# Kernel tuning notes

Hardware: AMD Instinct MI355X
Metric: run time of the kernel (lower is better)

## Reference

```python
import jax, jax.numpy as jnp
import numpy as np

N = 128       # HiPPO order
BATCH = 2
L = 2048      # max_length / sequence length
GBT_ALPHA = 0.5
STEP = 1.0


def _legs_transition(n_order):
    """HiPPO-LegS transition matrices A (N,N), B (N,1) as in TransMatrix(measure='legs')."""
    q = np.arange(n_order, dtype=np.float64)
    col, row = np.meshgrid(q, q)
    r = 2 * q + 1
    M = -(np.where(row >= col, r, 0.0) - np.diag(q))   # lower-tri + diag
    T = np.sqrt(2 * q + 1)
    A = (T[:, None] * M) / T[None, :]                  # T @ M @ inv(T)
    B = T[:, None]
    return A.astype(np.float32), B.astype(np.float32)


def setup_inputs() -> dict:
    key = jax.random.key(0)
    f = jax.random.normal(key, (BATCH, L, 1), dtype=jnp.float32)
    A_np, B_np = _legs_transition(N)
    return {
        "f": f,
        "A": jnp.asarray(A_np),
        "B": jnp.asarray(B_np),
        "C": jnp.ones((N, 1), dtype=jnp.float32),
        "D": jnp.zeros((1,), dtype=jnp.float32),
    }


def _discretize(A, B, step, alpha):
    """Generalized bilinear transform (alpha=0.5 -> bilinear)."""
    I = jnp.eye(A.shape[0], dtype=A.dtype)
    ss = 1.0 / step
    p1 = I - ss * alpha * A
    Ad = jnp.linalg.solve(p1, I + ss * (1.0 - alpha) * A)
    Bd = jnp.linalg.solve(p1, ss * B)
    return Ad, Bd


def reference(f, A, B, C, D):
    """HiPPO lti recurrence (verbose=False): returns (c_final, y_seq).
    c_final: (batch, 1, N); y_seq: (batch, L, N, N)."""
    n = A.shape[0]
    Ad, Bd = _discretize(A, B, STEP, GBT_ALPHA)          # (N,N), (N,1)
    c0 = jnp.zeros((f.shape[0], 1, n), dtype=f.dtype)     # init_state default
    f_t_first = jnp.swapaxes(f, 0, 1)                     # (L, batch, 1)

    def step(c, f_t):
        # c: (batch, 1, N), f_t: (batch, 1)
        c_new = c @ Ad.T + Bd.T * f_t[:, :, None]         # (batch, 1, N)
        # faithful to source: y_k = C @ c_k + D * f_k  ->  outer product (N,N)
        y = jnp.einsum('nm,bmk->bnk', C, c_new) + (D * f_t)[:, :, None]
        return c_new, y

    c_fin, ys = jax.lax.scan(step, c0, f_t_first)         # ys: (L, batch, N, N)
    ys = jnp.swapaxes(ys, 0, 1)                           # (batch, L, N, N)
    return c_fin, ys
```

## Files before the change

### kernel.cpp

```cpp
#include <hip/hip_runtime.h>
#include <math.h>

#define NSTATE 128
#define LSEQ   2048
#define NBATCH 2

typedef float f32x4 __attribute__((ext_vector_type(4)));

#define WS_MB0  0
#define WS_V    16384

__device__ __forceinline__ void solve_AdBd(float* __restrict__ Ads,
                                           float* __restrict__ Bds,
                                           const double* __restrict__ u,
                                           const double* __restrict__ invd,
                                           int tid) {
    if (tid > 128) return;
    int j = tid;
    double S = 0.0;
    double uj = (j < 128) ? u[j] : 0.0;
    for (int i = 0; i < 128; ++i) {
        double ui = u[i];
        double b;
        if (j == 128)      b = ui;
        else if (i < j)    b = 0.0;
        else if (i == j)   b = 1.0 - 0.5 * (j + 1);
        else               b = -0.5 * ui * uj;
        double x = (b - 0.5 * ui * S) * invd[i];
        S += ui * x;
        if (j == 128) Bds[i] = (float)x;
        else          Ads[i * 132 + j] = (float)x;
    }
}

__device__ __forceinline__ void chain_run(const float4 a[8], float4 vr[8],
                                          float* __restrict__ vb,
                                          int n, int h, int steps,
                                          float* __restrict__ Vst, int vstride,
                                          float* __restrict__ Mst) {
    for (int s = 1; s <= steps; ++s) {
        float s0 = 0.f, s1 = 0.f, s2 = 0.f, s3 = 0.f;
        #pragma unroll
        for (int q = 0; q < 8; ++q) {
            s0 = fmaf(a[q].x, vr[q].x, s0);
            s1 = fmaf(a[q].y, vr[q].y, s1);
            s2 = fmaf(a[q].z, vr[q].z, s2);
            s3 = fmaf(a[q].w, vr[q].w, s3);
        }
        float p = (s0 + s1) + (s2 + s3);
        p += __shfl_xor(p, 1);
        p += __shfl_xor(p, 2);
        float* cur = vb + (s & 1) * 144;
        if (h == 0) {
            cur[36 * (n >> 5) + (n & 31)] = p;
            if (Vst) Vst[s * vstride + n] = p;
            if (Mst && s == steps) Mst[n * 128] = p;
        }
        __syncthreads();
        const float4* vv = (const float4*)(cur + 36 * h);
        #pragma unroll
        for (int q = 0; q < 8; ++q) vr[q] = vv[q];
    }
}

__global__ __launch_bounds__(512) void k_pow2(float* __restrict__ M,
                                              float* __restrict__ V) {
    __shared__ float Ads[128 * 132];
    __shared__ float Bds[132];
    __shared__ double u[128], invd[128];
    __shared__ float vb[2 * 144];
    int tid = threadIdx.x, blk = blockIdx.x;
    if (tid < 128) { u[tid] = sqrt(2.0 * tid + 1.0); invd[tid] = 1.0 / (1.0 + 0.5 * (tid + 1)); }
    __syncthreads();
    solve_AdBd(Ads, Bds, u, invd, tid);
    __syncthreads();

    int n = tid >> 2, h = tid & 3;
    float4 a[8];
    const float4* Ar = (const float4*)(Ads + n * 132 + 32 * h);
    #pragma unroll
    for (int q = 0; q < 8; ++q) a[q] = Ar[q];
    float4 vr[8];
    if (blk == 128) {
        if (tid < 128) V[tid] = Bds[tid];
        const float4* Bv = (const float4*)(Bds + 32 * h);
        #pragma unroll
        for (int q = 0; q < 8; ++q) vr[q] = Bv[q];
        chain_run(a, vr, vb, n, h, 31, V, 128, nullptr);
    } else {
        #pragma unroll
        for (int q = 0; q < 8; ++q) {
            vr[q].x = (32 * h + 4 * q + 0 == blk) ? 1.f : 0.f;
            vr[q].y = (32 * h + 4 * q + 1 == blk) ? 1.f : 0.f;
            vr[q].z = (32 * h + 4 * q + 2 == blk) ? 1.f : 0.f;
            vr[q].w = (32 * h + 4 * q + 3 == blk) ? 1.f : 0.f;
        }
        chain_run(a, vr, vb, n, h, 32, nullptr, 0, M + blk);
    }
}

__global__ __launch_bounds__(512) void k_tails2(const float* __restrict__ M,
                                                float* __restrict__ V) {
    __shared__ float Ads[128 * 132];
    __shared__ float Bds[132];
    __shared__ double u[128], invd[128];
    __shared__ float vb[2 * 144];
    int tid = threadIdx.x, c = blockIdx.x + 1;
    if (tid < 128) { u[tid] = sqrt(2.0 * tid + 1.0); invd[tid] = 1.0 / (1.0 + 0.5 * (tid + 1)); }
    __syncthreads();
    solve_AdBd(Ads, Bds, u, invd, tid);
    __syncthreads();

    int n = tid >> 2, h = tid & 3;
    float4 am[8], aa[8], vr[8];
    const float4* Mr = (const float4*)(M + n * 128 + 32 * h);
    #pragma unroll
    for (int q = 0; q < 8; ++q) am[q] = Mr[q];
    const float4* Ar = (const float4*)(Ads + n * 132 + 32 * h);
    #pragma unroll
    for (int q = 0; q < 8; ++q) aa[q] = Ar[q];
    const float4* Bv = (const float4*)(Bds + 32 * h);
    #pragma unroll
    for (int q = 0; q < 8; ++q) vr[q] = Bv[q];

    chain_run(am, vr, vb, n, h, c, nullptr, 0, nullptr);
    float* Vrow = V + (size_t)c * 32 * 128;
    if (n == 0) {
        #pragma unroll
        for (int q = 0; q < 8; ++q) ((float4*)Vrow)[8 * h + q] = vr[q];
    }
    __syncthreads();
    chain_run(aa, vr, vb, n, h, 31, Vrow, 128, nullptr);
}

__global__ __launch_bounds__(512) void k_convwrite(const float* __restrict__ f,
                                                   const float* __restrict__ V,
                                                   float* __restrict__ out) {
    int b = blockIdx.x, tile = blockIdx.y;
    int t0 = tile * 8;
    int Dtot = t0 + 8;
    __shared__ float fL[2080];
    __shared__ float red[4][8][128];
    int tid = threadIdx.x;
    if (tid < 15) fL[tid] = 0.f;
    for (int x = tid; x < Dtot; x += 512) fL[15 + x] = f[b * LSEQ + x];
    __syncthreads();

    int k = tid & 127, h = tid >> 7;
    float acc[8];
    #pragma unroll
    for (int i = 0; i < 8; ++i) acc[i] = 0.f;

    int nblk = (Dtot + 15) >> 4;
    for (int ib = h; ib < nblk; ib += 4) {
        int dbase = ib << 4;
        int foff = t0 - dbase;
        float F[24];
        const f32x4* fv = (const f32x4*)(fL + foff);
        #pragma unroll
        for (int q = 0; q < 6; ++q) {
            f32x4 t4 = fv[q];
            F[4 * q] = t4.x; F[4 * q + 1] = t4.y; F[4 * q + 2] = t4.z; F[4 * q + 3] = t4.w;
        }
        const float* Vp = V + (size_t)dbase * 128 + k;
        #pragma unroll
        for (int dd = 0; dd < 16; ++dd) {
            float w = Vp[dd * 128];
            #pragma unroll
            for (int i = 0; i < 8; ++i)
                acc[i] = fmaf(w, F[15 + i - dd], acc[i]);
        }
    }

    #pragma unroll
    for (int i = 0; i < 8; ++i) red[h][i][k] = acc[i];
    __syncthreads();
    if (tid < 128) {
        #pragma unroll
        for (int i = 0; i < 8; ++i) {
            float s = red[0][i][tid] + red[1][i][tid] + red[2][i][tid] + red[3][i][tid];
            red[0][i][tid] = s;
        }
    }
    __syncthreads();

    const f32x4* outv = (const f32x4*)&red[0][0][0];
    int k32 = tid & 31, r0 = tid >> 5;
    float* ysb = out + 256 + ((size_t)(b * LSEQ + t0)) * 16384;
    #pragma unroll
    for (int t = 0; t < 8; ++t) {
        f32x4 v = outv[t * 32 + k32];
        float* yst = ysb + (size_t)t * 16384 + k32 * 4;
        #pragma unroll
        for (int p = 0; p < 8; ++p) {
            int n = p * 16 + r0;
            __builtin_nontemporal_store(v, (f32x4*)(yst + n * 128));
        }
    }
    if (tile == 255 && tid < 32)
        *(f32x4*)(out + b * 128 + tid * 4) = outv[7 * 32 + tid];
}

extern "C" void kernel_launch(void* const* d_in, const int* in_sizes, int n_in,
                              void* d_out, int out_size, void* d_ws, size_t ws_size,
                              hipStream_t stream) {
    const float* f = (const float*)d_in[0];
    float* ws   = (float*)d_ws;
    float* M32  = ws + WS_MB0;
    float* V    = ws + WS_V;
    float* out  = (float*)d_out;

    k_pow2  <<<129, 512, 0, stream>>>(M32, V);
    k_tails2<<<63,  512, 0, stream>>>(M32, V);
    dim3 cw(2, 256);
    k_convwrite<<<cw, 512, 0, stream>>>(f, V, out);
}
```

Before: 342.0 us.

## Fuse matrix-power and tail kernels with flag sync; pair convolution tiles

Merges the power-generation and tail-chain kernels into one 192-block launch. The tail blocks spin on per-column release/acquire flags until all 128 matrix-power columns are written, which removes a kernel boundary and lets independent work overlap. The convolution/write kernel now pairs a short tile with its long mirror tile per block, halving the block count and balancing the triangular workload. The flags are never reset between calls, so later calls can read stale flags; the tail blocks also rely on all blocks being resident at once.

After: 815.2 us. 138% more time.

```diff
diff --git a/kernel.cpp b/kernel.cpp
--- a/kernel.cpp
+++ b/kernel.cpp
@@ -1,14 +1,15 @@
 #include <hip/hip_runtime.h>
 #include <math.h>
 
-#define NSTATE 128
 #define LSEQ   2048
 #define NBATCH 2
+#define MAGIC  0x13572468u
 
 typedef float f32x4 __attribute__((ext_vector_type(4)));
 
-#define WS_MB0  0
-#define WS_V    16384
+#define WS_MB0   0
+#define WS_V     16384
+#define WS_FLAGM 278528
 
 __device__ __forceinline__ void solve_AdBd(float* __restrict__ Ads,
                                            float* __restrict__ Bds,
@@ -63,8 +64,9 @@
     }
 }
 
-__global__ __launch_bounds__(512) void k_pow2(float* __restrict__ M,
-                                              float* __restrict__ V) {
+__global__ __launch_bounds__(512) void k_vgen(float* __restrict__ M,
+                                              float* __restrict__ V,
+                                              unsigned* __restrict__ flagM) {
     __shared__ float Ads[128 * 132];
     __shared__ float Bds[132];
     __shared__ double u[128], invd[128];
@@ -76,18 +78,13 @@
     __syncthreads();
 
     int n = tid >> 2, h = tid & 3;
-    float4 a[8];
+    float4 aa[8];
     const float4* Ar = (const float4*)(Ads + n * 132 + 32 * h);
     #pragma unroll
-    for (int q = 0; q < 8; ++q) a[q] = Ar[q];
-    float4 vr[8];
-    if (blk == 128) {
-        if (tid < 128) V[tid] = Bds[tid];
-        const float4* Bv = (const float4*)(Bds + 32 * h);
-        #pragma unroll
-        for (int q = 0; q < 8; ++q) vr[q] = Bv[q];
-        chain_run(a, vr, vb, n, h, 31, V, 128, nullptr);
-    } else {
+    for (int q = 0; q < 8; ++q) aa[q] = Ar[q];
+
+    if (blk < 128) {
+        float4 vr[8];
         #pragma unroll
         for (int q = 0; q < 8; ++q) {
             vr[q].x = (32 * h + 4 * q + 0 == blk) ? 1.f : 0.f;
@@ -95,66 +92,67 @@
             vr[q].z = (32 * h + 4 * q + 2 == blk) ? 1.f : 0.f;
             vr[q].w = (32 * h + 4 * q + 3 == blk) ? 1.f : 0.f;
         }
-        chain_run(a, vr, vb, n, h, 32, nullptr, 0, M + blk);
-    }
-}
-
-__global__ __launch_bounds__(512) void k_tails2(const float* __restrict__ M,
-                                                float* __restrict__ V) {
-    __shared__ float Ads[128 * 132];
-    __shared__ float Bds[132];
-    __shared__ double u[128], invd[128];
-    __shared__ float vb[2 * 144];
-    int tid = threadIdx.x, c = blockIdx.x + 1;
-    if (tid < 128) { u[tid] = sqrt(2.0 * tid + 1.0); invd[tid] = 1.0 / (1.0 + 0.5 * (tid + 1)); }
-    __syncthreads();
-    solve_AdBd(Ads, Bds, u, invd, tid);
-    __syncthreads();
-
-    int n = tid >> 2, h = tid & 3;
-    float4 am[8], aa[8], vr[8];
-    const float4* Mr = (const float4*)(M + n * 128 + 32 * h);
-    #pragma unroll
-    for (int q = 0; q < 8; ++q) am[q] = Mr[q];
-    const float4* Ar = (const float4*)(Ads + n * 132 + 32 * h);
-    #pragma unroll
-    for (int q = 0; q < 8; ++q) aa[q] = Ar[q];
-    const float4* Bv = (const float4*)(Bds + 32 * h);
-    #pragma unroll
-    for (int q = 0; q < 8; ++q) vr[q] = Bv[q];
-
-    chain_run(am, vr, vb, n, h, c, nullptr, 0, nullptr);
-    float* Vrow = V + (size_t)c * 32 * 128;
-    if (n == 0) {
-        #pragma unroll
-        for (int q = 0; q < 8; ++q) ((float4*)Vrow)[8 * h + q] = vr[q];
-    }
-    __syncthreads();
-    chain_run(aa, vr, vb, n, h, 31, Vrow, 128, nullptr);
-}
-
-__global__ __launch_bounds__(512) void k_convwrite(const float* __restrict__ f,
-                                                   const float* __restrict__ V,
-                                                   float* __restrict__ out) {
-    int b = blockIdx.x, tile = blockIdx.y;
-    int t0 = tile * 8;
-    int Dtot = t0 + 8;
+        chain_run(aa, vr, vb, n, h, 32, nullptr, 0, M + blk);
+        __syncthreads();
+        if (tid == 0) {
+            __threadfence();
+            __hip_atomic_store(flagM + blk, MAGIC, __ATOMIC_RELEASE, __HIP_MEMORY_SCOPE_AGENT);
+        }
+    } else if (blk == 128) {
+        if (tid < 128) V[tid] = Bds[tid];
+        float4 vr[8];
+        const float4* Bv = (const float4*)(Bds + 32 * h);
+        #pragma unroll
+        for (int q = 0; q < 8; ++q) vr[q] = Bv[q];
+        chain_run(aa, vr, vb, n, h, 31, V, 128, nullptr);
+    } else {
+        int c = blk - 128;
+        float4 vr[8];
+        const float4* Bv = (const float4*)(Bds + 32 * h);
+        #pragma unroll
+        for (int q = 0; q < 8; ++q) vr[q] = Bv[q];
+        for (int j = 0; j < 128; ++j)
+            while (__hip_atomic_load(flagM + j, __ATOMIC_ACQUIRE, __HIP_MEMORY_SCOPE_AGENT) != MAGIC)
+                __builtin_amdgcn_s_sleep(2);
+        __syncthreads();
+        float4 am[8];
+        const float4* Mr = (const float4*)(M + n * 128 + 32 * h);
+        #pragma unroll
+        for (int q = 0; q < 8; ++q) am[q] = Mr[q];
+        chain_run(am, vr, vb, n, h, c, nullptr, 0, nullptr);
+        float* Vrow = V + (size_t)c * 32 * 128;
+        if (n == 0) {
+            #pragma unroll
+            for (int q = 0; q < 8; ++q) ((float4*)Vrow)[8 * h + q] = vr[q];
+        }
+        __syncthreads();
+        chain_run(aa, vr, vb, n, h, 31, Vrow, 128, nullptr);
+    }
+}
+
+__global__ __launch_bounds__(512) void k_convwrite2(const float* __restrict__ f,
+                                                    const float* __restrict__ V,
+                                                    float* __restrict__ out) {
+    int b = blockIdx.x, p = blockIdx.y;
+    int t0A = p * 8, t0B = (255 - p) * 8;
+    int DtotB = t0B + 8;
     __shared__ float fL[2080];
-    __shared__ float red[4][8][128];
+    __shared__ float redA[4][8][128];
+    __shared__ float redB[4][8][128];
     int tid = threadIdx.x;
     if (tid < 15) fL[tid] = 0.f;
-    for (int x = tid; x < Dtot; x += 512) fL[15 + x] = f[b * LSEQ + x];
+    for (int x = tid; x < DtotB; x += 512) fL[15 + x] = f[b * LSEQ + x];
     __syncthreads();
 
     int k = tid & 127, h = tid >> 7;
-    float acc[8];
-    #pragma unroll
-    for (int i = 0; i < 8; ++i) acc[i] = 0.f;
-
-    int nblk = (Dtot + 15) >> 4;
-    for (int ib = h; ib < nblk; ib += 4) {
+    float accA[8], accB[8];
+    #pragma unroll
+    for (int i = 0; i < 8; ++i) { accA[i] = 0.f; accB[i] = 0.f; }
+
+    int nblkA = (t0A + 23) >> 4;
+    for (int ib = h; ib < nblkA; ib += 4) {
         int dbase = ib << 4;
-        int foff = t0 - dbase;
+        int foff = t0A - dbase;
         float F[24];
         const f32x4* fv = (const f32x4*)(fL + foff);
         #pragma unroll
@@ -168,37 +166,60 @@
             float w = Vp[dd * 128];
             #pragma unroll
             for (int i = 0; i < 8; ++i)
-                acc[i] = fmaf(w, F[15 + i - dd], acc[i]);
-        }
-    }
-
-    #pragma unroll
-    for (int i = 0; i < 8; ++i) red[h][i][k] = acc[i];
+                accA[i] = fmaf(w, F[15 + i - dd], accA[i]);
+        }
+    }
+    int nblkB = (t0B + 23) >> 4;
+    for (int ib = h; ib < nblkB; ib += 4) {
+        int dbase = ib << 4;
+        int foff = t0B - dbase;
+        float F[24];
+        const f32x4* fv = (const f32x4*)(fL + foff);
+        #pragma unroll
+        for (int q = 0; q < 6; ++q) {
+            f32x4 t4 = fv[q];
+            F[4 * q] = t4.x; F[4 * q + 1] = t4.y; F[4 * q + 2] = t4.z; F[4 * q + 3] = t4.w;
+        }
+        const float* Vp = V + (size_t)dbase * 128 + k;
+        #pragma unroll
+        for (int dd = 0; dd < 16; ++dd) {
+            float w = Vp[dd * 128];
+            #pragma unroll
+            for (int i = 0; i < 8; ++i)
+                accB[i] = fmaf(w, F[15 + i - dd], accB[i]);
+        }
+    }
+
+    #pragma unroll
+    for (int i = 0; i < 8; ++i) { redA[h][i][k] = accA[i]; redB[h][i][k] = accB[i]; }
     __syncthreads();
     if (tid < 128) {
         #pragma unroll
         for (int i = 0; i < 8; ++i) {
-            float s = red[0][i][tid] + red[1][i][tid] + red[2][i][tid] + red[3][i][tid];
-            red[0][i][tid] = s;
-        }
-    }
-    __syncthreads();
-
-    const f32x4* outv = (const f32x4*)&red[0][0][0];
+            redA[0][i][tid] = redA[0][i][tid] + redA[1][i][tid] + redA[2][i][tid] + redA[3][i][tid];
+            redB[0][i][tid] = redB[0][i][tid] + redB[1][i][tid] + redB[2][i][tid] + redB[3][i][tid];
+        }
+    }
+    __syncthreads();
+
+    const f32x4* outA = (const f32x4*)&redA[0][0][0];
+    const f32x4* outB = (const f32x4*)&redB[0][0][0];
     int k32 = tid & 31, r0 = tid >> 5;
-    float* ysb = out + 256 + ((size_t)(b * LSEQ + t0)) * 16384;
+    float* ysA = out + 256 + ((size_t)(b * LSEQ + t0A)) * 16384 + k32 * 4;
+    float* ysB = out + 256 + ((size_t)(b * LSEQ + t0B)) * 16384 + k32 * 4;
     #pragma unroll
     for (int t = 0; t < 8; ++t) {
-        f32x4 v = outv[t * 32 + k32];
-        float* yst = ysb + (size_t)t * 16384 + k32 * 4;
-        #pragma unroll
-        for (int p = 0; p < 8; ++p) {
-            int n = p * 16 + r0;
-            __builtin_nontemporal_store(v, (f32x4*)(yst + n * 128));
-        }
-    }
-    if (tile == 255 && tid < 32)
-        *(f32x4*)(out + b * 128 + tid * 4) = outv[7 * 32 + tid];
+        f32x4 vA = outA[t * 32 + k32];
+        f32x4 vB = outB[t * 32 + k32];
+        #pragma unroll
+        for (int q = 0; q < 8; ++q) {
+            int n = q * 16 + r0;
+            __builtin_nontemporal_store(vA, (f32x4*)(ysA + (size_t)t * 16384 + n * 128));
+            __builtin_nontemporal_store(vB, (f32x4*)(ysB + (size_t)t * 16384 + n * 128));
+        }
+    }
+    if (p == 0 && tid < 32)
+        *(f32x4*)(out + b * 128 + tid * 4) = outB[7 * 32 + tid];
 }
 
 extern "C" void kernel_launch(void* const* d_in, const int* in_sizes, int n_in,
@@ -208,10 +229,10 @@
     float* ws   = (float*)d_ws;
     float* M32  = ws + WS_MB0;
     float* V    = ws + WS_V;
+    unsigned* flagM = (unsigned*)(ws + WS_FLAGM);
     float* out  = (float*)d_out;
 
-    k_pow2  <<<129, 512, 0, stream>>>(M32, V);
-    k_tails2<<<63,  512, 0, stream>>>(M32, V);
-    dim3 cw(2, 256);
-    k_convwrite<<<cw, 512, 0, stream>>>(f, V, out);
-}
+    k_vgen<<<192, 512, 0, stream>>>(M32, V, flagM);
+    dim3 cw(2, 128);
+    k_convwrite2<<<cw, 512, 0, stream>>>(f, V, out);
+}
```
